# Kernel optimization log

Measured on AMD Instinct MI355X. Metric: run time of the kernel, lower is better.

The kernel has to match this reference:

```python
import jax, jax.numpy as jnp
import numpy as np

DN = ('NCDHW', 'OIDHW', 'NCDHW')

def conv(x, w, stride=1):
    k = w.shape[-1]
    pad = 'VALID' if k == 2 else 'SAME'  # ks=2,s=2 Minkowski offsets {0,1}; ks=3 centered; ks=1 pointwise
    return jax.lax.conv_general_dilated(x, w, (stride,) * 3, pad, dimension_numbers=DN)

def masked_bn(x, m, eps=1e-5):
    # BatchNorm over occupied voxels only (MinkowskiBatchNorm semantics); affine is identity at init.
    cnt = jnp.maximum(jnp.sum(m), 1.0)
    mean = jnp.sum(x * m, axis=(0, 2, 3, 4)) / cnt
    xc = (x - mean.reshape(1, -1, 1, 1, 1)) * m  # also zeroes unoccupied sites
    var = jnp.sum(xc * xc, axis=(0, 2, 3, 4)) / cnt
    return xc * jax.lax.rsqrt(var + eps).reshape(1, -1, 1, 1, 1)

def downmask(m):
    B, _, D, H, W = m.shape
    return m.reshape(B, 1, D // 2, 2, H // 2, 2, W // 2, 2).max(axis=(3, 5, 7))

def cbr(x, m, w):
    return jax.nn.relu(masked_bn(conv(x, w), m))

def res(x, m, wa, wb, wsk):
    y = masked_bn(conv(jax.nn.relu(masked_bn(conv(x, wa), m)), wb), m)
    sk = x if wsk is None else masked_bn(conv(x, wsk), m)
    return jax.nn.relu(y + sk)

def stage(x, m, wd, wa1, wb1, wsk, wa2, wb2):
    m2 = downmask(m)  # output coord set of ks=2,s=2 sparse conv
    x = jax.nn.relu(masked_bn(conv(x, wd, 2), m2))  # BasicConvolutionBlock
    x = res(x, m2, wa1, wb1, wsk)
    x = res(x, m2, wa2, wb2, None)
    return x, m2

def _forward(feats, mask, ws0, ws1, d1, a11, b11, a12, b12, d2, a21, b21, k2, a22, b22,
             d3, a31, b31, k3, a32, b32, d4, a41, b41, k4, a42, b42):
    m = mask
    x = cbr(feats * m, m, ws0)
    x = cbr(x, m, ws1)
    x, m = stage(x, m, d1, a11, b11, None, a12, b12)   # 32 -> 32 (identity skip)
    x, m = stage(x, m, d2, a21, b21, k2, a22, b22)     # 32 -> 64
    x, m = stage(x, m, d3, a31, b31, k3, a32, b32)     # 64 -> 128
    x, m = stage(x, m, d4, a41, b41, k4, a42, b42)     # 128 -> 256
    return x

def setup_inputs() -> dict:
    key = jax.random.key(0)
    ks = jax.random.split(key, 28)
    def W(k, o, i, s):
        return jax.random.normal(k, (o, i, s, s, s), jnp.float32) / np.sqrt(i * s ** 3)
    feats = jax.random.normal(ks[0], (2, 3, 64, 64, 64), jnp.float32)
    mask = (jax.random.uniform(ks[1], (2, 1, 64, 64, 64)) < 0.1).astype(jnp.float32)
    return dict(
        feats=feats * mask, mask=mask,
        ws0=W(ks[2], 32, 3, 3), ws1=W(ks[3], 32, 32, 3),
        d1=W(ks[4], 32, 32, 2), a11=W(ks[5], 32, 32, 3), b11=W(ks[6], 32, 32, 3),
        a12=W(ks[7], 32, 32, 3), b12=W(ks[8], 32, 32, 3),
        d2=W(ks[9], 32, 32, 2), a21=W(ks[10], 64, 32, 3), b21=W(ks[11], 64, 64, 3),
        k2=W(ks[12], 64, 32, 1), a22=W(ks[13], 64, 64, 3), b22=W(ks[14], 64, 64, 3),
        d3=W(ks[15], 64, 64, 2), a31=W(ks[16], 128, 64, 3), b31=W(ks[17], 128, 128, 3),
        k3=W(ks[18], 128, 64, 1), a32=W(ks[19], 128, 128, 3), b32=W(ks[20], 128, 128, 3),
        d4=W(ks[21], 128, 128, 2), a41=W(ks[22], 256, 128, 3), b41=W(ks[23], 256, 256, 3),
        k4=W(ks[24], 256, 128, 1), a42=W(ks[25], 256, 256, 3), b42=W(ks[26], 256, 256, 3))

def reference(feats, mask, ws0, ws1, d1, a11, b11, a12, b12, d2, a21, b21, k2, a22, b22,
              d3, a31, b31, k3, a32, b32, d4, a41, b41, k4, a42, b42):
    return _forward(feats, mask, ws0, ws1, d1, a11, b11, a12, b12, d2, a21, b21, k2, a22, b22,
                    d3, a31, b31, k3, a32, b32, d4, a41, b41, k4, a42, b42)
```

## Files before the change

kernel.cpp:

```cpp
#include <hip/hip_runtime.h>

#define BLK 256

static inline int gup(long work) { return (int)((work + BLK - 1) / BLK); }

__device__ inline bool occ_pred(const float* mask, const int* fmap,
                                int i, int DHW, int Ho, int Wo, int mode) {
  if (mode == 0) return mask[i] > 0.f;
  int b = i / DHW, sp = i - b * DHW;
  int HW = Ho * Wo;
  int z = sp / HW, r = sp - z * HW, y = r / Wo, x = r - y * Wo;
  int Hi = 2 * Ho, Wi = 2 * Wo;
  const int* mb = fmap + b * 8 * DHW;
  int base = ((2 * z) * Hi + 2 * y) * Wi + 2 * x;
  bool occ = false;
  for (int dz = 0; dz < 2; dz++)
    for (int dy = 0; dy < 2; dy++)
      for (int dx = 0; dx < 2; dx++)
        occ |= mb[base + dz * Hi * Wi + dy * Wi + dx] >= 0;
  return occ;
}

__global__ __launch_bounds__(1024) void cnt_k(const float* mask, const int* fmap,
    int* bcnt, int DHW, int Ho, int Wo, int mode, int total) {
  int i = blockIdx.x * 1024 + threadIdx.x;
  bool occ = (i < total) && occ_pred(mask, fmap, i, DHW, Ho, Wo, mode);
  unsigned long long bal = __ballot(occ);
  __shared__ int ws[16];
  int lane = threadIdx.x & 63, wid = threadIdx.x >> 6;
  if (lane == 0) ws[wid] = __popcll(bal);
  __syncthreads();
  if (threadIdx.x == 0) {
    int a = 0;
    for (int w = 0; w < 16; w++) a += ws[w];
    bcnt[blockIdx.x] = a;
  }
}

__global__ __launch_bounds__(1024) void scan_k(int* bcnt, int nb, int* cnt) {
  __shared__ int sh[1024];
  int t = threadIdx.x;
  int v = (t < nb) ? bcnt[t] : 0;
  sh[t] = v;
  __syncthreads();
  for (int o = 1; o < 1024; o <<= 1) {
    int u = (t >= o) ? sh[t - o] : 0;
    __syncthreads();
    sh[t] += u;
    __syncthreads();
  }
  if (t < nb) bcnt[t] = sh[t] - v;
  if (t == 0) *cnt = sh[1023];
}

__global__ __launch_bounds__(1024) void emit_k(const float* mask, const int* fmap,
    const int* boff, int* map, int* list, int DHW, int Ho, int Wo, int mode, int total) {
  int i = blockIdx.x * 1024 + threadIdx.x;
  bool occ = (i < total) && occ_pred(mask, fmap, i, DHW, Ho, Wo, mode);
  unsigned long long bal = __ballot(occ);
  int lane = threadIdx.x & 63, wid = threadIdx.x >> 6;
  __shared__ int wcnt[16], woff[16];
  if (lane == 0) wcnt[wid] = __popcll(bal);
  __syncthreads();
  if (threadIdx.x == 0) {
    int a = boff[blockIdx.x];
    for (int w = 0; w < 16; w++) { woff[w] = a; a += wcnt[w]; }
  }
  __syncthreads();
  if (i < total) {
    if (occ) {
      int p = woff[wid] + __popcll(bal & ((1ull << lane) - 1ull));
      map[i] = p; list[p] = i;
    } else map[i] = -1;
  }
}

__global__ __launch_bounds__(1024) void compact1_k(const int* __restrict__ fmap,
    int* __restrict__ map, int* __restrict__ list, int* __restrict__ cntp,
    int Do, int Ho, int Wo) {
  int DHW = Do * Ho * Wo, total = 2 * DHW;
  int tid = threadIdx.x, lane = tid & 63, wid = tid >> 6;
  bool occ = (tid < total) && occ_pred(nullptr, fmap, tid, DHW, Ho, Wo, 1);
  unsigned long long bal = __ballot(occ);
  __shared__ int wcnt[16], woff[16];
  if (lane == 0) wcnt[wid] = __popcll(bal);
  __syncthreads();
  if (tid == 0) {
    int a = 0;
    for (int w = 0; w < 16; w++) { woff[w] = a; a += wcnt[w]; }
    *cntp = a;
  }
  __syncthreads();
  if (tid < total) {
    if (occ) {
      int p = woff[wid] + __popcll(bal & ((1ull << lane) - 1ull));
      map[tid] = p; list[p] = tid;
    } else map[tid] = -1;
  }
}

__global__ __launch_bounds__(256) void csr_both_k(
    const int* __restrict__ list, const int* __restrict__ map,
    const int* __restrict__ cntp, const int* __restrict__ fmap,
    int* __restrict__ csr27, int* __restrict__ csr8,
    int D, int H, int W, int do8) {
  int n = *cntp;
  int DHW = D * H * W;
  for (int v = blockIdx.x * 256 + threadIdx.x; v < n; v += gridDim.x * 256) {
    int idx = list[v];
    int b = idx / DHW, sp = idx - b * DHW;
    int z = sp / (H * W), r = sp - z * H * W, y = r / W, x = r - y * W;
    const int* mb = map + b * DHW;
    int* e = csr27 + (long)v * 28;
    int cnt = 0;
    for (int k = 0; k < 27; k++) {
      int dz = k / 9 - 1, dy = (k / 3) % 3 - 1, dx = k % 3 - 1;
      int zz = z + dz, yy = y + dy, xx = x + dx;
      if ((unsigned)zz >= (unsigned)D || (unsigned)yy >= (unsigned)H ||
          (unsigned)xx >= (unsigned)W) continue;
      int j = mb[(zz * H + yy) * W + xx];
      if (j >= 0) e[++cnt] = (k << 24) | j;
    }
    e[0] = cnt;
    if (do8) {
      int Hi = 2 * H, Wi = 2 * W;
      const int* fb = fmap + b * 8 * DHW;
      int* e8 = csr8 + (long)v * 9;
      int c8 = 0;
      for (int k = 0; k < 8; k++) {
        int dz = k >> 2, dy = (k >> 1) & 1, dx = k & 1;
        int j = fb[((2 * z + dz) * Hi + 2 * y + dy) * Wi + 2 * x + dx];
        if (j >= 0) e8[++c8] = (k << 24) | j;
      }
      e8[0] = c8;
    }
  }
}

struct WAll {
  const float* src[25];
  float* dst[25];
  int O[25], I[25], K[25];
  int sb[26];
};

__global__ __launch_bounds__(256) void wtr_all_k(WAll wa) {
  int b = blockIdx.x;
  int w = 0;
  while (w < 24 && b >= wa.sb[w + 1]) ++w;
  int O = wa.O[w], I = wa.I[w], K = wa.K[w];
  int I4 = (I + 3) >> 2;
  long tot = (long)K * I4 * O * 4;
  long t = (long)(b - wa.sb[w]) * 256 + threadIdx.x;
  if (t >= tot) return;
  int e = (int)(t & 3); long r = t >> 2;
  int co = (int)(r % O); long r2 = r / O;
  int ci4 = (int)(r2 % I4); int k = (int)(r2 / I4);
  int ci = 4 * ci4 + e;
  wa.dst[w][t] = (ci < I) ? wa.src[w][((long)co * I + ci) * K + k] : 0.f;
}

__global__ void gather0_k(const float* __restrict__ feats, const int* __restrict__ list,
                          const int* __restrict__ cntp, float* __restrict__ rows, int DHW) {
  int n = *cntp;
  int t = blockIdx.x * BLK + threadIdx.x;
  if (t >= n * 4) return;
  int vox = t >> 2, c = t & 3;
  int idx = list[vox]; int b = idx / DHW, sp = idx - b * DHW;
  rows[t] = (c < 3) ? feats[(b * 3 + c) * DHW + sp] : 0.f;
}

template <int CIN, int COUT, int ES, bool PRE>
__global__ __launch_bounds__(256) void convc_k(
    const float* __restrict__ fin, const float* __restrict__ wt,
    float* __restrict__ fout, const int* __restrict__ csr,
    const int* __restrict__ cntp, const int* __restrict__ pcntp,
    const float* __restrict__ pslot, float* __restrict__ slot) {
  constexpr int CL = COUT / 2, G = 256 / CL, C4 = CIN / 4;
  constexpr int EST = (ES > 0) ? ES : 1;
  constexpr int CPD = PRE ? CIN : 4;
  __shared__ float4 rbuf[G * C4];
  __shared__ int se[G * EST];
  __shared__ float aP[CPD], bP[CPD];
  __shared__ float sA[256], sB[256];
  __shared__ int scmax;
  int n = *cntp;
  int vb = blockIdx.x * G;
  if (vb >= n) return;
  int tid = threadIdx.x;
  if constexpr (PRE) {
    int np = *pcntp;
    float c = fmaxf((float)np, 1.f);
    for (int ch = tid; ch < CIN; ch += 256) {
      float s = 0.f, q = 0.f;
      #pragma unroll
      for (int r = 0; r < 4; r++) { s += pslot[r * 512 + ch]; q += pslot[r * 512 + 256 + ch]; }
      float mean = s / c, var = fmaxf(q / c - mean * mean, 0.f);
      float a = rsqrtf(var + 1e-5f);
      aP[ch] = a; bP[ch] = -mean * a;
    }
  }
  int cmax;
  if constexpr (ES > 0) {
    if (tid == 0) scmax = 0;
    __syncthreads();
    for (int u = tid; u < G * ES; u += 256) {
      int v = vb + u / ES;
      int e = (v < n) ? csr[(long)vb * ES + u] : 0;
      se[u] = e;
      if ((u % ES) == 0) atomicMax(&scmax, e);
    }
    __syncthreads();
    cmax = scmax;
  } else {
    __syncthreads();
    cmax = 1;
  }
  int cl = tid % CL, g = tid / CL;
  int v = vb + g;
  bool alive = v < n;
  float a0 = 0.f, a1 = 0.f;
  const float4* fin4 = (const float4*)fin;
  const float4* w4 = (const float4*)wt;
  for (int i = 1; i <= cmax; i++) {
    __syncthreads();
    for (int u = tid; u < G * C4; u += 256) {
      int gg = u / C4, c4 = u - gg * C4;
      int pj = -1;
      if constexpr (ES > 0) {
        if (vb + gg < n && i <= se[gg * EST]) pj = se[gg * EST + i];
      } else {
        if (vb + gg < n) pj = vb + gg;
      }
      float4 val = make_float4(0.f, 0.f, 0.f, 0.f);
      if (pj >= 0) {
        int j = pj & 0xFFFFFF;
        val = fin4[(long)j * C4 + c4];
        if constexpr (PRE) {
          int ch = 4 * c4;
          val.x = fmaxf(val.x * aP[ch] + bP[ch], 0.f);
          val.y = fmaxf(val.y * aP[ch + 1] + bP[ch + 1], 0.f);
          val.z = fmaxf(val.z * aP[ch + 2] + bP[ch + 2], 0.f);
          val.w = fmaxf(val.w * aP[ch + 3] + bP[ch + 3], 0.f);
        }
      }
      rbuf[u] = val;
    }
    __syncthreads();
    int pj;
    if constexpr (ES > 0) {
      pj = (alive && i <= se[g * EST]) ? se[g * EST + i] : -1;
    } else {
      pj = alive ? v : -1;
    }
    if (pj >= 0) {
      int k = pj >> 24;
      const float4* wk = w4 + (long)k * C4 * COUT + cl;
      #pragma unroll 8
      for (int c4 = 0; c4 < C4; c4++) {
        float4 rv = rbuf[g * C4 + c4];
        float4 w0 = wk[c4 * COUT];
        float4 w1 = wk[c4 * COUT + CL];
        a0 += rv.x * w0.x + rv.y * w0.y + rv.z * w0.z + rv.w * w0.w;
        a1 += rv.x * w1.x + rv.y * w1.y + rv.z * w1.z + rv.w * w1.w;
      }
    }
  }
  if (alive) {
    fout[(long)v * COUT + cl] = a0;
    fout[(long)v * COUT + cl + CL] = a1;
  }
  __syncthreads();
  sA[tid] = alive ? a0 : 0.f; sB[tid] = alive ? a1 : 0.f;
  __syncthreads();
  for (int o = 128; o >= CL; o >>= 1) {
    if (tid < o) { sA[tid] += sA[tid + o]; sB[tid] += sB[tid + o]; }
    __syncthreads();
  }
  float s0 = 0.f, s1 = 0.f;
  if (tid < CL) { s0 = sA[tid]; s1 = sB[tid]; }
  __syncthreads();
  sA[tid] = alive ? a0 * a0 : 0.f; sB[tid] = alive ? a1 * a1 : 0.f;
  __syncthreads();
  for (int o = 128; o >= CL; o >>= 1) {
    if (tid < o) { sA[tid] += sA[tid + o]; sB[tid] += sB[tid + o]; }
    __syncthreads();
  }
  if (tid < CL) {
    float* sl = slot + (blockIdx.x & 3) * 512;
    atomicAdd(&sl[tid], s0);
    atomicAdd(&sl[tid + CL], s1);
    atomicAdd(&sl[256 + tid], sA[tid]);
    atomicAdd(&sl[256 + tid + CL], sB[tid]);
  }
}

template <int CIN, int COUT, int NS, bool PRE>
__global__ __launch_bounds__(256) void convs_k(
    const float* __restrict__ fin, const float* __restrict__ wt,
    float* __restrict__ fout, const int* __restrict__ csr,
    const int* __restrict__ cntp, const int* __restrict__ pcntp,
    const float* __restrict__ pslot) {
  constexpr int CL = COUT / 2, G = 256 / CL, C4 = CIN / 4;
  constexpr int CPD = PRE ? CIN : 4;
  __shared__ float4 rbuf[G * C4];
  __shared__ int se[G * 28];
  __shared__ float aP[CPD], bP[CPD];
  __shared__ int scmax;
  int n = *cntp;
  int vb = blockIdx.x * G;
  if (vb >= n) return;
  int tid = threadIdx.x;
  int y = blockIdx.y;
  if constexpr (PRE) {
    int np = *pcntp;
    float c = fmaxf((float)np, 1.f);
    for (int ch = tid; ch < CIN; ch += 256) {
      float s = 0.f, q = 0.f;
      #pragma unroll
      for (int r = 0; r < 4; r++) { s += pslot[r * 512 + ch]; q += pslot[r * 512 + 256 + ch]; }
      float mean = s / c, var = fmaxf(q / c - mean * mean, 0.f);
      float a = rsqrtf(var + 1e-5f);
      aP[ch] = a; bP[ch] = -mean * a;
    }
  }
  if (tid == 0) scmax = 0;
  __syncthreads();
  for (int u = tid; u < G * 28; u += 256) {
    int v = vb + u / 28;
    int e = (v < n) ? csr[(long)vb * 28 + u] : 0;
    se[u] = e;
    if ((u % 28) == 0) atomicMax(&scmax, e);
  }
  __syncthreads();
  int cmax = scmax;
  int cl = tid % CL, g = tid / CL;
  int v = vb + g;
  bool alive = v < n;
  float a0 = 0.f, a1 = 0.f;
  const float4* fin4 = (const float4*)fin;
  const float4* w4 = (const float4*)wt;
  for (int i = 1 + y; i <= cmax; i += NS) {
    __syncthreads();
    for (int u = tid; u < G * C4; u += 256) {
      int gg = u / C4, c4 = u - gg * C4;
      int pj = -1;
      if (vb + gg < n && i <= se[gg * 28]) pj = se[gg * 28 + i];
      float4 val = make_float4(0.f, 0.f, 0.f, 0.f);
      if (pj >= 0) {
        int j = pj & 0xFFFFFF;
        val = fin4[(long)j * C4 + c4];
        if constexpr (PRE) {
          int ch = 4 * c4;
          val.x = fmaxf(val.x * aP[ch] + bP[ch], 0.f);
          val.y = fmaxf(val.y * aP[ch + 1] + bP[ch + 1], 0.f);
          val.z = fmaxf(val.z * aP[ch + 2] + bP[ch + 2], 0.f);
          val.w = fmaxf(val.w * aP[ch + 3] + bP[ch + 3], 0.f);
        }
      }
      rbuf[u] = val;
    }
    __syncthreads();
    int pj = (alive && i <= se[g * 28]) ? se[g * 28 + i] : -1;
    if (pj >= 0) {
      int k = pj >> 24;
      const float4* wk = w4 + (long)k * C4 * COUT + cl;
      #pragma unroll 8
      for (int c4 = 0; c4 < C4; c4++) {
        float4 rv = rbuf[g * C4 + c4];
        float4 w0 = wk[c4 * COUT];
        float4 w1 = wk[c4 * COUT + CL];
        a0 += rv.x * w0.x + rv.y * w0.y + rv.z * w0.z + rv.w * w0.w;
        a1 += rv.x * w1.x + rv.y * w1.y + rv.z * w1.z + rv.w * w1.w;
      }
    }
  }
  if (alive) {
    atomicAdd(&fout[(long)v * COUT + cl], a0);
    atomicAdd(&fout[(long)v * COUT + cl + CL], a1);
  }
}

template <int C>
__global__ __launch_bounds__(BLK) void bnred_k(const float* __restrict__ rows,
    const int* __restrict__ cntp, float* __restrict__ slot) {
  int n = *cntp;
  long tot = (long)n * C;
  int tid = threadIdx.x;
  float s = 0.f, s2 = 0.f;
  for (long t = (long)blockIdx.x * BLK + tid; t < tot; t += (long)gridDim.x * BLK) {
    float v = rows[t]; s += v; s2 += v * v;
  }
  __shared__ float sh[BLK], sh2[BLK];
  sh[tid] = s; sh2[tid] = s2;
  __syncthreads();
  for (int o = BLK / 2; o >= C; o >>= 1) {
    if (tid < o) { sh[tid] += sh[tid + o]; sh2[tid] += sh2[tid + o]; }
    __syncthreads();
  }
  if (tid < C) { atomicAdd(&slot[tid], sh[tid]); atomicAdd(&slot[256 + tid], sh2[tid]); }
}

template <int C, int MODE>
__global__ __launch_bounds__(256) void skipapp_k(
    const float* __restrict__ x, const float* __restrict__ y,
    const float* __restrict__ s1, const float* __restrict__ s2,
    const int* __restrict__ cntp, float* __restrict__ out) {
  __shared__ float a1_[C], b1_[C], a2_[C], b2_[C];
  int n = *cntp;
  int tid = threadIdx.x;
  float cnt = fmaxf((float)n, 1.f);
  for (int c = tid; c < C; c += 256) {
    float s = 0.f, q = 0.f;
    #pragma unroll
    for (int r = 0; r < 4; r++) { s += s1[r * 512 + c]; q += s1[r * 512 + 256 + c]; }
    float mean = s / cnt, var = fmaxf(q / cnt - mean * mean, 0.f);
    float a = rsqrtf(var + 1e-5f);
    a1_[c] = a; b1_[c] = -mean * a;
    if (MODE != 2) {
      s = 0.f; q = 0.f;
      #pragma unroll
      for (int r = 0; r < 4; r++) { s += s2[r * 512 + c]; q += s2[r * 512 + 256 + c]; }
      mean = s / cnt; var = fmaxf(q / cnt - mean * mean, 0.f);
      a = rsqrtf(var + 1e-5f);
      a2_[c] = a; b2_[c] = -mean * a;
    }
  }
  __syncthreads();
  constexpr int C4 = C / 4;
  long tot = (long)n * C4;
  for (long t = (long)blockIdx.x * 256 + tid; t < tot; t += (long)gridDim.x * 256) {
    int c = 4 * (int)(t % C4);
    float4 xv = ((const float4*)x)[t];
    float4 yv = ((const float4*)y)[t];
    float4 o;
    o.x = xv.x * a1_[c] + b1_[c];
    o.y = xv.y * a1_[c + 1] + b1_[c + 1];
    o.z = xv.z * a1_[c + 2] + b1_[c + 2];
    o.w = xv.w * a1_[c + 3] + b1_[c + 3];
    if (MODE == 0) {
      o.x += yv.x * a2_[c] + b2_[c];
      o.y += yv.y * a2_[c + 1] + b2_[c + 1];
      o.z += yv.z * a2_[c + 2] + b2_[c + 2];
      o.w += yv.w * a2_[c + 3] + b2_[c + 3];
    } else if (MODE == 1) {
      o.x += fmaxf(yv.x * a2_[c] + b2_[c], 0.f);
      o.y += fmaxf(yv.y * a2_[c + 1] + b2_[c + 1], 0.f);
      o.z += fmaxf(yv.z * a2_[c + 2] + b2_[c + 2], 0.f);
      o.w += fmaxf(yv.w * a2_[c + 3] + b2_[c + 3], 0.f);
    } else {
      o.x += yv.x; o.y += yv.y; o.z += yv.z; o.w += yv.w;
    }
    o.x = fmaxf(o.x, 0.f); o.y = fmaxf(o.y, 0.f);
    o.z = fmaxf(o.z, 0.f); o.w = fmaxf(o.w, 0.f);
    ((float4*)out)[t] = o;
  }
}

__global__ void scatter_k(const float* __restrict__ rows, const int* __restrict__ list,
                          const int* __restrict__ cntp, float* __restrict__ out, int DHW) {
  int n = *cntp;
  int t = blockIdx.x * BLK + threadIdx.x;
  if (t >= n * 256) return;
  int vox = t >> 8, c = t & 255;
  int idx = list[vox]; int b = idx / DHW, sp = idx - b * DHW;
  out[(b * 256 + c) * DHW + sp] = rows[t];
}

#define CAP0 81920
#define CAP1 57344
#define CAP2 8192
#define CAP3 1024
#define CAP4 128

extern "C" void kernel_launch(void* const* d_in, const int* in_sizes, int n_in,
                              void* d_out, int out_size, void* d_ws, size_t ws_size,
                              hipStream_t stream) {
  const float* feats = (const float*)d_in[0];
  const float* mask0 = (const float*)d_in[1];

  char* p = (char*)d_ws;
  auto alloc = [&](size_t bytes) { char* r = p; p += (bytes + 255) & ~255ull; return r; };

  const int tab[25][4] = {
    {2, 32, 3, 27},  {3, 32, 32, 27}, {4, 32, 32, 8},  {5, 32, 32, 27}, {6, 32, 32, 27},
    {7, 32, 32, 27}, {8, 32, 32, 27}, {9, 32, 32, 8},  {10, 64, 32, 27},{11, 64, 64, 27},
    {12, 64, 32, 1}, {13, 64, 64, 27},{14, 64, 64, 27},{15, 64, 64, 8}, {16, 128, 64, 27},
    {17, 128, 128, 27},{18, 128, 64, 1},{19, 128, 128, 27},{20, 128, 128, 27},
    {21, 128, 128, 8},{22, 256, 128, 27},{23, 256, 256, 27},{24, 256, 128, 1},
    {25, 256, 256, 27},{26, 256, 256, 27},
  };
  WAll wa;
  float* wT[27] = {nullptr};
  int blk = 0;
  for (int i = 0; i < 25; i++) {
    int idx = tab[i][0], O = tab[i][1], I = tab[i][2], K = tab[i][3];
    int I4 = (I + 3) / 4;
    long sz = (long)K * I4 * O * 4;
    wT[idx] = (float*)alloc((size_t)sz * 4);
    wa.src[i] = (const float*)d_in[idx]; wa.dst[i] = wT[idx];
    wa.O[i] = O; wa.I[i] = I; wa.K[i] = K;
    wa.sb[i] = blk; blk += (int)((sz + 255) / 256);
  }
  wa.sb[25] = blk;

  int* map0 = (int*)alloc(524288 * 4);
  int* list0 = (int*)alloc((size_t)CAP0 * 4);
  int* map1 = (int*)alloc(65536 * 4);
  int* list1 = (int*)alloc((size_t)CAP1 * 4);
  int* map2 = (int*)alloc(8192 * 4);
  int* list2 = (int*)alloc(8192 * 4);
  int* map3 = (int*)alloc(1024 * 4);
  int* list3 = (int*)alloc(1024 * 4);
  int* map4 = (int*)alloc(128 * 4);
  int* list4 = (int*)alloc(128 * 4);
  int* bcnt = (int*)alloc(1024 * 4);
  int* cnts = (int*)alloc(32 * 4);
  int* c27_0 = (int*)alloc((size_t)CAP0 * 28 * 4);
  int* c27_1 = (int*)alloc((size_t)CAP1 * 28 * 4);
  int* c8_1  = (int*)alloc((size_t)CAP1 * 9 * 4);
  int* c27_2 = (int*)alloc((size_t)CAP2 * 28 * 4);
  int* c8_2  = (int*)alloc((size_t)CAP2 * 9 * 4);
  int* c27_3 = (int*)alloc((size_t)CAP3 * 28 * 4);
  int* c8_3  = (int*)alloc((size_t)CAP3 * 9 * 4);
  int* c27_4 = (int*)alloc((size_t)CAP4 * 28 * 4);
  int* c8_4  = (int*)alloc((size_t)CAP4 * 9 * 4);
  float* stats = (float*)alloc(25 * 2048 * 4);
  float* G0  = (float*)alloc((size_t)CAP0 * 4 * 4);
  float* F0a = (float*)alloc((size_t)CAP0 * 32 * 4);
  float* F0b = (float*)alloc((size_t)CAP0 * 32 * 4);
  float *R1[4], *R2[4];
  for (int i = 0; i < 4; i++) R1[i] = (float*)alloc((size_t)CAP1 * 32 * 4);
  for (int i = 0; i < 4; i++) R2[i] = (float*)alloc((size_t)CAP2 * 64 * 4);
  size_t z3sz = (size_t)CAP3 * 128 * 4 * 6 + (size_t)CAP4 * 256 * 4 * 6;
  float* Z3 = (float*)alloc(z3sz);
  float* R3[6], *R4[6];
  for (int i = 0; i < 6; i++) R3[i] = Z3 + (size_t)i * CAP3 * 128;
  for (int i = 0; i < 6; i++) R4[i] = Z3 + (size_t)6 * CAP3 * 128 + (size_t)i * CAP4 * 256;

  hipMemsetAsync(stats, 0, 25 * 2048 * 4, stream);
  hipMemsetAsync(Z3, 0, z3sz, stream);
  hipMemsetAsync(d_out, 0, (size_t)out_size * 4, stream);

  wtr_all_k<<<blk, 256, 0, stream>>>(wa);

  int* n0 = cnts + 0; int* n1 = cnts + 1; int* n2 = cnts + 2;
  int* n3 = cnts + 3; int* n4 = cnts + 4;

  cnt_k<<<512, 1024, 0, stream>>>(mask0, nullptr, bcnt, 262144, 64, 64, 0, 524288);
  scan_k<<<1, 1024, 0, stream>>>(bcnt, 512, n0);
  emit_k<<<512, 1024, 0, stream>>>(mask0, nullptr, bcnt, map0, list0, 262144, 64, 64, 0, 524288);
  gather0_k<<<gup((long)CAP0 * 4), BLK, 0, stream>>>(feats, list0, n0, G0, 262144);
  csr_both_k<<<512, 256, 0, stream>>>(list0, map0, n0, nullptr, c27_0, nullptr, 64, 64, 64, 0);

  cnt_k<<<64, 1024, 0, stream>>>(nullptr, map0, bcnt, 32768, 32, 32, 1, 65536);
  scan_k<<<1, 1024, 0, stream>>>(bcnt, 64, n1);
  emit_k<<<64, 1024, 0, stream>>>(nullptr, map0, bcnt, map1, list1, 32768, 32, 32, 1, 65536);
  csr_both_k<<<256, 256, 0, stream>>>(list1, map1, n1, map0, c27_1, c8_1, 32, 32, 32, 1);

  cnt_k<<<8, 1024, 0, stream>>>(nullptr, map1, bcnt, 4096, 16, 16, 1, 8192);
  scan_k<<<1, 1024, 0, stream>>>(bcnt, 8, n2);
  emit_k<<<8, 1024, 0, stream>>>(nullptr, map1, bcnt, map2, list2, 4096, 16, 16, 1, 8192);
  csr_both_k<<<32, 256, 0, stream>>>(list2, map2, n2, map1, c27_2, c8_2, 16, 16, 16, 1);

  compact1_k<<<1, 1024, 0, stream>>>(map2, map3, list3, n3, 8, 8, 8);
  csr_both_k<<<4, 256, 0, stream>>>(list3, map3, n3, map2, c27_3, c8_3, 8, 8, 8, 1);

  compact1_k<<<1, 1024, 0, stream>>>(map3, map4, list4, n4, 4, 4, 4);
  csr_both_k<<<1, 256, 0, stream>>>(list4, map4, n4, map3, c27_4, c8_4, 4, 4, 4, 1);

  auto slot = [&](int i) { return stats + (size_t)i * 2048; };
  auto bgrid = [&](long cap, int C) { long g = (cap * C / 4 + 255) / 256; return (int)(g > 2048 ? 2048 : g); };

  {
    int g = (CAP0 + 15) / 16;
    convc_k<4, 32, 28, false><<<g, 256, 0, stream>>>(G0, wT[2], F0a, c27_0, n0, nullptr, nullptr, slot(0));
    convc_k<32, 32, 28, true><<<g, 256, 0, stream>>>(F0a, wT[3], F0b, c27_0, n0, n0, slot(0), slot(1));
  }

  {
    int g = (CAP1 + 15) / 16, ag = bgrid(CAP1, 32);
    convc_k<32, 32, 9, true><<<g, 256, 0, stream>>>(F0b, wT[4], R1[0], c8_1, n1, n0, slot(1), slot(2));
    convc_k<32, 32, 28, true><<<g, 256, 0, stream>>>(R1[0], wT[5], R1[1], c27_1, n1, n1, slot(2), slot(3));
    convc_k<32, 32, 28, true><<<g, 256, 0, stream>>>(R1[1], wT[6], R1[2], c27_1, n1, n1, slot(3), slot(4));
    skipapp_k<32, 1><<<ag, 256, 0, stream>>>(R1[2], R1[0], slot(4), slot(2), n1, R1[3]);
    convc_k<32, 32, 28, false><<<g, 256, 0, stream>>>(R1[3], wT[7], R1[1], c27_1, n1, nullptr, nullptr, slot(5));
    convc_k<32, 32, 28, true><<<g, 256, 0, stream>>>(R1[1], wT[8], R1[2], c27_1, n1, n1, slot(5), slot(6));
    skipapp_k<32, 2><<<ag, 256, 0, stream>>>(R1[2], R1[3], slot(6), nullptr, n1, R1[0]);
  }

  {
    int gP = (CAP2 + 15) / 16, gO = (CAP2 + 7) / 8, ag = bgrid(CAP2, 64);
    convc_k<32, 32, 9, false><<<gP, 256, 0, stream>>>(R1[0], wT[9], R2[0], c8_2, n2, nullptr, nullptr, slot(7));
    convc_k<32, 64, 28, true><<<gO, 256, 0, stream>>>(R2[0], wT[10], R2[1], c27_2, n2, n2, slot(7), slot(8));
    convc_k<64, 64, 28, true><<<gO, 256, 0, stream>>>(R2[1], wT[11], R2[2], c27_2, n2, n2, slot(8), slot(9));
    convc_k<32, 64, 0, true><<<gO, 256, 0, stream>>>(R2[0], wT[12], R2[3], nullptr, n2, n2, slot(7), slot(10));
    skipapp_k<64, 0><<<ag, 256, 0, stream>>>(R2[2], R2[3], slot(9), slot(10), n2, R2[1]);
    convc_k<64, 64, 28, false><<<gO, 256, 0, stream>>>(R2[1], wT[13], R2[0], c27_2, n2, nullptr, nullptr, slot(11));
    convc_k<64, 64, 28, true><<<gO, 256, 0, stream>>>(R2[0], wT[14], R2[2], c27_2, n2, n2, slot(11), slot(12));
    skipapp_k<64, 2><<<ag, 256, 0, stream>>>(R2[2], R2[1], slot(12), nullptr, n2, R2[3]);
  }

  {
    int gP = (CAP3 + 7) / 8, gO = (CAP3 + 3) / 4, ag = bgrid(CAP3, 128);
    int rO = gup((long)CAP3 * 128); if (rO > 512) rO = 512;
    convc_k<64, 64, 9, false><<<gP, 256, 0, stream>>>(R2[3], wT[15], R3[0], c8_3, n3, nullptr, nullptr, slot(13));
    convs_k<64, 128, 4, true><<<dim3(gO, 4), 256, 0, stream>>>(R3[0], wT[16], R3[1], c27_3, n3, n3, slot(13));
    bnred_k<128><<<rO, BLK, 0, stream>>>(R3[1], n3, slot(14));
    convs_k<128, 128, 4, true><<<dim3(gO, 4), 256, 0, stream>>>(R3[1], wT[17], R3[2], c27_3, n3, n3, slot(14));
    bnred_k<128><<<rO, BLK, 0, stream>>>(R3[2], n3, slot(15));
    convc_k<64, 128, 0, true><<<gO, 256, 0, stream>>>(R3[0], wT[18], R3[3], nullptr, n3, n3, slot(13), slot(16));
    skipapp_k<128, 0><<<ag, 256, 0, stream>>>(R3[2], R3[3], slot(15), slot(16), n3, R3[1]);
    convs_k<128, 128, 4, false><<<dim3(gO, 4), 256, 0, stream>>>(R3[1], wT[19], R3[4], c27_3, n3, nullptr, nullptr);
    bnred_k<128><<<rO, BLK, 0, stream>>>(R3[4], n3, slot(17));
    convs_k<128, 128, 4, true><<<dim3(gO, 4), 256, 0, stream>>>(R3[4], wT[20], R3[5], c27_3, n3, n3, slot(17));
    bnred_k<128><<<rO, BLK, 0, stream>>>(R3[5], n3, slot(18));
    skipapp_k<128, 2><<<ag, 256, 0, stream>>>(R3[5], R3[1], slot(18), nullptr, n3, R3[0]);
  }

  {
    int gP = (CAP4 + 3) / 4, gO = (CAP4 + 1) / 2, ag = bgrid(CAP4, 256);
    int rO = gup((long)CAP4 * 256); if (rO > 512) rO = 512;
    convc_k<128, 128, 9, false><<<gP, 256, 0, stream>>>(R3[0], wT[21], R4[0], c8_4, n4, nullptr, nullptr, slot(19));
    convs_k<128, 256, 16, true><<<dim3(gO, 16), 256, 0, stream>>>(R4[0], wT[22], R4[1], c27_4, n4, n4, slot(19));
    bnred_k<256><<<rO, BLK, 0, stream>>>(R4[1], n4, slot(20));
    convs_k<256, 256, 16, true><<<dim3(gO, 16), 256, 0, stream>>>(R4[1], wT[23], R4[2], c27_4, n4, n4, slot(20));
    bnred_k<256><<<rO, BLK, 0, stream>>>(R4[2], n4, slot(21));
    convc_k<128, 256, 0, true><<<gO, 256, 0, stream>>>(R4[0], wT[24], R4[3], nullptr, n4, n4, slot(19), slot(22));
    skipapp_k<256, 0><<<ag, 256, 0, stream>>>(R4[2], R4[3], slot(21), slot(22), n4, R4[1]);
    convs_k<256, 256, 16, false><<<dim3(gO, 16), 256, 0, stream>>>(R4[1], wT[25], R4[4], c27_4, n4, nullptr, nullptr);
    bnred_k<256><<<rO, BLK, 0, stream>>>(R4[4], n4, slot(23));
    convs_k<256, 256, 16, true><<<dim3(gO, 16), 256, 0, stream>>>(R4[4], wT[26], R4[5], c27_4, n4, n4, slot(23));
    bnred_k<256><<<rO, BLK, 0, stream>>>(R4[5], n4, slot(24));
    skipapp_k<256, 2><<<ag, 256, 0, stream>>>(R4[5], R4[1], slot(24), nullptr, n4, R4[0]);
  }

  scatter_k<<<gup((long)CAP4 * 256), BLK, 0, stream>>>(R4[0], list4, n4, (float*)d_out, 64);
}
```

Before: 1.515 ms.

## Add offset-major sparse conv kernel staging weights in LDS with register-tiled outputs

```diff
diff --git a/kernel.cpp b/kernel.cpp
--- a/kernel.cpp
+++ b/kernel.cpp
@@ -122,6 +122,7 @@
       if (j >= 0) e[++cnt] = (k << 24) | j;
     }
     e[0] = cnt;
+    for (int s = cnt + 1; s <= 27; s++) e[s] = -1;
     if (do8) {
       int Hi = 2 * H, Wi = 2 * W;
       const int* fb = fmap + b * 8 * DHW;
@@ -133,6 +134,7 @@
         if (j >= 0) e8[++c8] = (k << 24) | j;
       }
       e8[0] = c8;
+      for (int s = c8 + 1; s <= 8; s++) e8[s] = -1;
     }
   }
 }
@@ -168,6 +170,129 @@
   int vox = t >> 2, c = t & 3;
   int idx = list[vox]; int b = idx / DHW, sp = idx - b * DHW;
   rows[t] = (c < 3) ? feats[(b * 3 + c) * DHW + sp] : 0.f;
+}
+
+template <int CIN, int COUT, int CPT, int VX, int NT, bool PRE>
+__global__ __launch_bounds__(256) void convk_k(
+    const float* __restrict__ fin, const float* __restrict__ wt,
+    float* __restrict__ fout, const int* __restrict__ csr,
+    const int* __restrict__ cntp, const int* __restrict__ pcntp,
+    const float* __restrict__ pslot, float* __restrict__ slot) {
+  constexpr int CL = COUT / CPT;
+  constexpr int G = 256 / CL;
+  constexpr int VT = G * VX;
+  constexpr int C4 = CIN / 4;
+  constexpr int WSZ = C4 * COUT;
+  __shared__ int jtab[VT * NT];
+  __shared__ float4 rbuf[VT * C4];
+  __shared__ float4 wbuf[WSZ];
+  __shared__ float aP[PRE ? CIN : 4], bP[PRE ? CIN : 4];
+  __shared__ float swA[256], swB[256];
+  int n = *cntp;
+  int vb = blockIdx.x * VT;
+  if (vb >= n) return;
+  int tid = threadIdx.x;
+  if constexpr (PRE) {
+    int np = *pcntp;
+    float c = fmaxf((float)np, 1.f);
+    for (int ch = tid; ch < CIN; ch += 256) {
+      float s = 0.f, q = 0.f;
+      #pragma unroll
+      for (int r = 0; r < 4; r++) { s += pslot[r * 512 + ch]; q += pslot[r * 512 + 256 + ch]; }
+      float mean = s / c, var = fmaxf(q / c - mean * mean, 0.f);
+      float a = rsqrtf(var + 1e-5f);
+      aP[ch] = a; bP[ch] = -mean * a;
+    }
+  }
+  for (int u = tid; u < VT * NT; u += 256) jtab[u] = -1;
+  __syncthreads();
+  for (int u = tid; u < VT * (NT + 1); u += 256) {
+    int v = u / (NT + 1), s = u - v * (NT + 1);
+    if (s > 0 && vb + v < n) {
+      int e = csr[(long)(vb + v) * (NT + 1) + s];
+      if (e >= 0) jtab[v * NT + (e >> 24)] = e & 0xFFFFFF;
+    }
+  }
+  int cl = tid % CL, g = tid / CL, vg = g * VX;
+  float acc[VX][CPT];
+  #pragma unroll
+  for (int vx = 0; vx < VX; vx++)
+    #pragma unroll
+    for (int m = 0; m < CPT; m++) acc[vx][m] = 0.f;
+  const float4* fin4 = (const float4*)fin;
+  const float4* w4 = (const float4*)wt;
+  for (int k = 0; k < NT; k++) {
+    __syncthreads();
+    for (int u = tid; u < WSZ; u += 256) wbuf[u] = w4[(long)k * WSZ + u];
+    for (int u = tid; u < VT * C4; u += 256) {
+      int v = u / C4, c4 = u - v * C4;
+      int j = jtab[v * NT + k];
+      float4 val = make_float4(0.f, 0.f, 0.f, 0.f);
+      if (j >= 0) {
+        val = fin4[(long)j * C4 + c4];
+        if constexpr (PRE) {
+          int ch = 4 * c4;
+          val.x = fmaxf(val.x * aP[ch] + bP[ch], 0.f);
+          val.y = fmaxf(val.y * aP[ch + 1] + bP[ch + 1], 0.f);
+          val.z = fmaxf(val.z * aP[ch + 2] + bP[ch + 2], 0.f);
+          val.w = fmaxf(val.w * aP[ch + 3] + bP[ch + 3], 0.f);
+        }
+      }
+      rbuf[u] = val;
+    }
+    __syncthreads();
+    #pragma unroll
+    for (int c4 = 0; c4 < C4; c4++) {
+      float4 w_[CPT];
+      #pragma unroll
+      for (int m = 0; m < CPT; m++) w_[m] = wbuf[c4 * COUT + cl + m * CL];
+      #pragma unroll
+      for (int vx = 0; vx < VX; vx++) {
+        float4 rv = rbuf[(vg + vx) * C4 + c4];
+        #pragma unroll
+        for (int m = 0; m < CPT; m++)
+          acc[vx][m] += rv.x * w_[m].x + rv.y * w_[m].y + rv.z * w_[m].z + rv.w * w_[m].w;
+      }
+    }
+  }
+  #pragma unroll
+  for (int vx = 0; vx < VX; vx++) {
+    int v = vb + vg + vx;
+    if (v < n) {
+      #pragma unroll
+      for (int m = 0; m < CPT; m++)
+        fout[(long)v * COUT + cl + m * CL] = acc[vx][m];
+    }
+  }
+  int lane = tid & 63, wid = tid >> 6;
+  #pragma unroll
+  for (int m = 0; m < CPT; m++) {
+    float ps = 0.f, pq = 0.f;
+    #pragma unroll
+    for (int vx = 0; vx < VX; vx++) { ps += acc[vx][m]; pq += acc[vx][m] * acc[vx][m]; }
+    #pragma unroll
+    for (int o = 32; o >= CL; o >>= 1) {
+      ps += __shfl_down(ps, o);
+      pq += __shfl_down(pq, o);
+    }
+    if (lane < CL) {
+      swA[(m * 4 + wid) * CL + lane] = ps;
+      swB[(m * 4 + wid) * CL + lane] = pq;
+    }
+  }
+  __syncthreads();
+  if (tid < COUT) {
+    int m = tid / CL, c2 = tid % CL;
+    float s = 0.f, q = 0.f;
+    #pragma unroll
+    for (int w = 0; w < 4; w++) {
+      s += swA[(m * 4 + w) * CL + c2];
+      q += swB[(m * 4 + w) * CL + c2];
+    }
+    float* sl = slot + (blockIdx.x & 3) * 512;
+    atomicAdd(&sl[tid], s);
+    atomicAdd(&sl[256 + tid], q);
+  }
 }
 
 template <int CIN, int COUT, int ES, bool PRE>
@@ -573,31 +698,31 @@
   auto bgrid = [&](long cap, int C) { long g = (cap * C / 4 + 255) / 256; return (int)(g > 2048 ? 2048 : g); };
 
   {
-    int g = (CAP0 + 15) / 16;
-    convc_k<4, 32, 28, false><<<g, 256, 0, stream>>>(G0, wT[2], F0a, c27_0, n0, nullptr, nullptr, slot(0));
-    convc_k<32, 32, 28, true><<<g, 256, 0, stream>>>(F0a, wT[3], F0b, c27_0, n0, n0, slot(0), slot(1));
+    int g = (CAP0 + 63) / 64;
+    convk_k<4, 32, 4, 2, 27, false><<<g, 256, 0, stream>>>(G0, wT[2], F0a, c27_0, n0, nullptr, nullptr, slot(0));
+    convk_k<32, 32, 4, 2, 27, true><<<g, 256, 0, stream>>>(F0a, wT[3], F0b, c27_0, n0, n0, slot(0), slot(1));
   }
 
   {
-    int g = (CAP1 + 15) / 16, ag = bgrid(CAP1, 32);
-    convc_k<32, 32, 9, true><<<g, 256, 0, stream>>>(F0b, wT[4], R1[0], c8_1, n1, n0, slot(1), slot(2));
-    convc_k<32, 32, 28, true><<<g, 256, 0, stream>>>(R1[0], wT[5], R1[1], c27_1, n1, n1, slot(2), slot(3));
-    convc_k<32, 32, 28, true><<<g, 256, 0, stream>>>(R1[1], wT[6], R1[2], c27_1, n1, n1, slot(3), slot(4));
+    int g = (CAP1 + 63) / 64, ag = bgrid(CAP1, 32);
+    convk_k<32, 32, 4, 2, 8, true><<<g, 256, 0, stream>>>(F0b, wT[4], R1[0], c8_1, n1, n0, slot(1), slot(2));
+    convk_k<32, 32, 4, 2, 27, true><<<g, 256, 0, stream>>>(R1[0], wT[5], R1[1], c27_1, n1, n1, slot(2), slot(3));
+    convk_k<32, 32, 4, 2, 27, true><<<g, 256, 0, stream>>>(R1[1], wT[6], R1[2], c27_1, n1, n1, slot(3), slot(4));
     skipapp_k<32, 1><<<ag, 256, 0, stream>>>(R1[2], R1[0], slot(4), slot(2), n1, R1[3]);
-    convc_k<32, 32, 28, false><<<g, 256, 0, stream>>>(R1[3], wT[7], R1[1], c27_1, n1, nullptr, nullptr, slot(5));
-    convc_k<32, 32, 28, true><<<g, 256, 0, stream>>>(R1[1], wT[8], R1[2], c27_1, n1, n1, slot(5), slot(6));
+    convk_k<32, 32, 4, 2, 27, false><<<g, 256, 0, stream>>>(R1[3], wT[7], R1[1], c27_1, n1, nullptr, nullptr, slot(5));
+    convk_k<32, 32, 4, 2, 27, true><<<g, 256, 0, stream>>>(R1[1], wT[8], R1[2], c27_1, n1, n1, slot(5), slot(6));
     skipapp_k<32, 2><<<ag, 256, 0, stream>>>(R1[2], R1[3], slot(6), nullptr, n1, R1[0]);
   }
 
   {
-    int gP = (CAP2 + 15) / 16, gO = (CAP2 + 7) / 8, ag = bgrid(CAP2, 64);
-    convc_k<32, 32, 9, false><<<gP, 256, 0, stream>>>(R1[0], wT[9], R2[0], c8_2, n2, nullptr, nullptr, slot(7));
-    convc_k<32, 64, 28, true><<<gO, 256, 0, stream>>>(R2[0], wT[10], R2[1], c27_2, n2, n2, slot(7), slot(8));
-    convc_k<64, 64, 28, true><<<gO, 256, 0, stream>>>(R2[1], wT[11], R2[2], c27_2, n2, n2, slot(8), slot(9));
-    convc_k<32, 64, 0, true><<<gO, 256, 0, stream>>>(R2[0], wT[12], R2[3], nullptr, n2, n2, slot(7), slot(10));
+    int g32 = (CAP2 + 31) / 32, ag = bgrid(CAP2, 64);
+    convk_k<32, 32, 4, 1, 8, false><<<g32, 256, 0, stream>>>(R1[0], wT[9], R2[0], c8_2, n2, nullptr, nullptr, slot(7));
+    convk_k<32, 64, 4, 2, 27, true><<<g32, 256, 0, stream>>>(R2[0], wT[10], R2[1], c27_2, n2, n2, slot(7), slot(8));
+    convk_k<64, 64, 4, 2, 27, true><<<g32, 256, 0, stream>>>(R2[1], wT[11], R2[2], c27_2, n2, n2, slot(8), slot(9));
+    convc_k<32, 64, 0, true><<<(CAP2 + 7) / 8, 256, 0, stream>>>(R2[0], wT[12], R2[3], nullptr, n2, n2, slot(7), slot(10));
     skipapp_k<64, 0><<<ag, 256, 0, stream>>>(R2[2], R2[3], slot(9), slot(10), n2, R2[1]);
-    convc_k<64, 64, 28, false><<<gO, 256, 0, stream>>>(R2[1], wT[13], R2[0], c27_2, n2, nullptr, nullptr, slot(11));
-    convc_k<64, 64, 28, true><<<gO, 256, 0, stream>>>(R2[0], wT[14], R2[2], c27_2, n2, n2, slot(11), slot(12));
+    convk_k<64, 64, 4, 2, 27, false><<<g32, 256, 0, stream>>>(R2[1], wT[13], R2[0], c27_2, n2, nullptr, nullptr, slot(11));
+    convk_k<64, 64, 4, 2, 27, true><<<g32, 256, 0, stream>>>(R2[0], wT[14], R2[2], c27_2, n2, n2, slot(11), slot(12));
     skipapp_k<64, 2><<<ag, 256, 0, stream>>>(R2[2], R2[1], slot(12), nullptr, n2, R2[3]);
   }
 
```

New measurement: 1.499 ms. No clear change (-1.1%).
